# Kernel optimization log

Hardware: AMD Instinct MI355X
Metric: run time of the kernel (lower is better)

Reference implementation:

```python
import jax, jax.numpy as jnp
import numpy as np

B, S, D, UNITS = 8, 2048, 512, 512

def setup_inputs() -> dict:
    key = jax.random.key(0)
    k1, k2, k3, k4, k5 = jax.random.split(key, 5)
    inputs = jax.random.normal(k1, (B, S, D), dtype=jnp.float32)
    scale = 1.0 / np.sqrt(D)
    Ww = jax.random.normal(k2, (D, UNITS), dtype=jnp.float32) * scale
    Wb = jnp.zeros((UNITS,), dtype=jnp.float32)
    Uw = jax.random.normal(k3, (D, UNITS), dtype=jnp.float32) * scale
    Ub = jnp.zeros((UNITS,), dtype=jnp.float32)
    return {"inputs": inputs, "Ww": Ww, "Wb": Wb, "Uw": Uw, "Ub": Ub}

def reference(inputs, Ww, Wb, Uw, Ub):
    # query/key projections: [B,S,units]
    query = jnp.einsum('bsd,du->bsu', inputs, Ww) + Wb
    key_ = jnp.einsum('bsd,du->bsu', inputs, Uw) + Ub
    # unscaled scores [B,S,S], softmax over last axis
    scores = jnp.einsum('bqu,bku->bqk', query, key_)
    attn = jax.nn.softmax(scores, axis=-1)
    # context uses raw inputs as values
    context = jnp.einsum('bqk,bkd->bqd', attn, inputs)
    return context
```

## Files before the change

kernel.cpp:

```cpp
#include <hip/hip_runtime.h>
#include <stdint.h>

#define B_ 8
#define S_ 2048
#define D_ 512
#define U_ 512
#define M_TOTAL (B_*S_)
#define NPROJ (2*U_)
#define QBLK 64
#define KVBLK 64
#define NIT (S_/KVBLK)

typedef __attribute__((ext_vector_type(8))) _Float16 f16x8;
typedef __attribute__((ext_vector_type(4))) float f32x4;

__device__ __forceinline__ uint16_t f2h(float f){
  return __builtin_bit_cast(uint16_t, (_Float16)f);
}

__device__ __forceinline__ void gload16(const void* g, void* l){
  __builtin_amdgcn_global_load_lds(
      (const __attribute__((address_space(1))) void*)g,
      (__attribute__((address_space(3))) void*)l, 16, 0, 0);
}

template<int ROWS>
__device__ __forceinline__ void stage_half(char* lbase, const uint16_t* __restrict__ gpanel,
                                           int ld, int wv, int lane){
  int r0 = wv*8 + (lane>>3);
  int gs = ((lane&7) ^ (r0&7)) << 3;
  gload16(gpanel + (size_t)r0*ld + gs, lbase + wv*1024);
  if constexpr (ROWS==128){
    gload16(gpanel + (size_t)(r0+64)*ld + gs, lbase + 8192 + wv*1024);
  }
}

__global__ __launch_bounds__(256) void prep_w(const float* __restrict__ Ww,
                                              const float* __restrict__ Uw,
                                              uint16_t* __restrict__ WT){
  int idx = blockIdx.x*256 + threadIdx.x;
  int u = idx >> 9;
  int d = idx & 511;
  float v = (u < U_) ? Ww[d*U_ + u] : Uw[d*U_ + (u-U_)];
  WT[idx] = f2h(v);
}

__global__ __launch_bounds__(256) void prep_x(const float* __restrict__ X,
                                              uint16_t* __restrict__ Xf,
                                              uint16_t* __restrict__ XT){
  __shared__ float tile[32][33];
  int b = blockIdx.z;
  int s0 = blockIdx.x * 32;
  int d0 = blockIdx.y * 32;
  int tid = threadIdx.x;
  int tr = tid >> 5;
  int tc = tid & 31;
  const float* Xb = X + (size_t)b*S_*D_;
#pragma unroll
  for (int i = 0; i < 32; i += 8){
    size_t off = (size_t)(s0+tr+i)*D_ + d0+tc;
    float v = Xb[off];
    tile[tr+i][tc] = v;
    Xf[(size_t)b*S_*D_ + off] = f2h(v);
  }
  __syncthreads();
  uint16_t* XTb = XT + (size_t)b*D_*S_;
#pragma unroll
  for (int i = 0; i < 32; i += 8)
    XTb[(size_t)(d0+tr+i)*S_ + s0+tc] = f2h(tile[tc][tr+i]);
}

__global__ __launch_bounds__(512, 2) void gemm_proj(
    const uint16_t* __restrict__ A, int lda,
    const uint16_t* __restrict__ Bp, int ldb,
    uint16_t* __restrict__ Qo, uint16_t* __restrict__ Ko,
    const float* __restrict__ biasW, const float* __restrict__ biasU,
    int KD)
{
  constexpr int BMH   = 128;
  constexpr int MFR   = 8;
  constexpr int AHALF = BMH*128;
  constexpr int BHALF = 128*128;
  constexpr int DSTR  = 2*AHALF + 2*BHALF;
  __shared__ __align__(16) char smem[2*DSTR];

  const int m0 = blockIdx.y * 256;
  const int n0 = blockIdx.x * 256;
  const uint16_t* Apan = A  + (size_t)m0*lda;
  const uint16_t* Bpan = Bp + (size_t)n0*ldb;

  const int t512 = threadIdx.x;
  const int wv   = t512 >> 6;
  const int lane = t512 & 63;
  const int wm   = wv >> 2;
  const int wn   = wv & 3;
  const int fr   = lane & 15;
  const int fg   = lane >> 4;
  const int sw   = fr & 7;

  const int NT = KD >> 6;

  auto Aslot = [&](int par, int h){ return smem + par*DSTR + h*AHALF; };
  auto Bslot = [&](int par, int h){ return smem + par*DSTR + 2*AHALF + h*BHALF; };

  stage_half<128>(Aslot(0,0), Apan,                   lda, wv, lane);
  stage_half<128>(Aslot(0,1), Apan + (size_t)128*lda, lda, wv, lane);
  stage_half<128>(Bslot(0,0), Bpan,                   ldb, wv, lane);
  stage_half<128>(Bslot(0,1), Bpan + (size_t)128*ldb, ldb, wv, lane);
  if (NT > 1)
    stage_half<128>(Aslot(1,0), Apan + 64,            lda, wv, lane);
  asm volatile("s_waitcnt vmcnt(2)" ::: "memory");
  __builtin_amdgcn_s_barrier();

  f32x4 acc[MFR][4];
#pragma unroll
  for (int i=0;i<MFR;i++)
#pragma unroll
    for (int j=0;j<4;j++) acc[i][j] = (f32x4){0.f,0.f,0.f,0.f};

  for (int t = 0; t < NT; ++t){
    const int p = t & 1;
    const char* myA = Aslot(p, wm);
    const char* myB = Bslot(p, wn>>1);
    f16x8 af[MFR];

    auto rdA = [&](int ks){
#pragma unroll
      for (int mf=0; mf<MFR; ++mf)
        af[mf] = *(const f16x8*)(myA + (mf*16+fr)*128 + (((ks<<2)|fg) ^ sw)*16);
    };
    auto rdB = [&](int ks, int nh, f16x8& b0, f16x8& b1){
      int rb = (wn&1)*64 + nh*32 + fr;
      b0 = *(const f16x8*)(myB + rb*128      + (((ks<<2)|fg) ^ sw)*16);
      b1 = *(const f16x8*)(myB + (rb+16)*128 + (((ks<<2)|fg) ^ sw)*16);
    };
    auto mm = [&](int nh, f16x8 b0, f16x8 b1){
      __builtin_amdgcn_s_setprio(1);
#pragma unroll
      for (int mf=0; mf<MFR; ++mf){
        acc[mf][nh*2]   = __builtin_amdgcn_mfma_f32_16x16x32_f16(af[mf], b0, acc[mf][nh*2],   0,0,0);
        acc[mf][nh*2+1] = __builtin_amdgcn_mfma_f32_16x16x32_f16(af[mf], b1, acc[mf][nh*2+1], 0,0,0);
      }
      __builtin_amdgcn_s_setprio(0);
    };

    f16x8 b0, b1;
    rdA(0); rdB(0, 0, b0, b1);
    if (t+1 < NT)
      stage_half<128>(Aslot(p^1,1), Apan + (size_t)128*lda + (t+1)*64, lda, wv, lane);
    __builtin_amdgcn_s_barrier();
    mm(0, b0, b1);
    __builtin_amdgcn_s_barrier();
    rdB(0, 1, b0, b1);
    if (t+1 < NT)
      stage_half<128>(Bslot(p^1,0), Bpan + (t+1)*64, ldb, wv, lane);
    __builtin_amdgcn_s_barrier();
    mm(1, b0, b1);
    __builtin_amdgcn_s_barrier();
    rdA(1); rdB(1, 0, b0, b1);
    if (t+1 < NT)
      stage_half<128>(Bslot(p^1,1), Bpan + (size_t)128*ldb + (t+1)*64, ldb, wv, lane);
    __builtin_amdgcn_s_barrier();
    mm(0, b0, b1);
    __builtin_amdgcn_s_barrier();
    rdB(1, 1, b0, b1);
    if (t+2 < NT)
      stage_half<128>(Aslot(p,0), Apan + (t+2)*64, lda, wv, lane);
    __builtin_amdgcn_s_barrier();
    mm(1, b0, b1);
    asm volatile("s_waitcnt vmcnt(2)" ::: "memory");
    __builtin_amdgcn_s_barrier();
  }

#pragma unroll
  for (int mf=0; mf<MFR; ++mf)
#pragma unroll
    for (int nf=0; nf<4; ++nf){
      int col  = n0 + wn*64 + nf*16 + fr;
      int rowb = m0 + wm*128 + mf*16 + fg*4;
      f32x4 a = acc[mf][nf];
      float bias = (col < U_) ? biasW[col] : biasU[col - U_];
      if (col < U_){
#pragma unroll
        for (int r=0;r<4;r++) Qo[(size_t)(rowb+r)*U_ + col] = f2h(a[r] + bias);
      } else {
#pragma unroll
        for (int r=0;r<4;r++) Ko[(size_t)(rowb+r)*U_ + col - U_] = f2h(a[r] + bias);
      }
    }
}

__global__ __launch_bounds__(512, 2) void flash_attn(
    const uint16_t* __restrict__ Qf,
    const uint16_t* __restrict__ Kf,
    const uint16_t* __restrict__ XT,
    float* __restrict__ Out)
{
  __shared__ __align__(16) uint16_t Ks[KVBLK][512];
  __shared__ __align__(16) uint16_t Vs[512][KVBLK];
  __shared__ __align__(16) float    Ss[QBLK][68];
  __shared__ __align__(16) uint16_t Ps[QBLK][KVBLK];
  __shared__ float m_s[QBLK], l_s[QBLK], f_s[QBLK];

  const int bid   = blockIdx.x;
  const int batch = bid & 7;
  const int mblk  = bid >> 3;
  const int s0    = mblk * QBLK;

  const int t    = threadIdx.x;
  const int wv   = t >> 6;
  const int lane = t & 63;
  const int fr   = lane & 15;
  const int fg   = lane >> 4;
  const int qg = wv >> 1;
  const int kh = wv & 1;
  const int wm = wv >> 2;
  const int wd = wv & 3;

  const uint16_t* Qrow = Qf + ((size_t)batch*S_ + s0)*U_;
  const uint16_t* Krow = Kf + (size_t)batch*S_*U_;
  const uint16_t* Vt   = XT + (size_t)batch*D_*S_;

  f16x8 qreg[16];
#pragma unroll
  for (int kk=0; kk<16; ++kk)
    qreg[kk] = *(const f16x8*)(Qrow + (size_t)(qg*16+fr)*U_ + kk*32 + fg*8);

  auto stageK = [&](int ti){
    const uint16_t* src = Krow + (size_t)(ti*KVBLK)*U_;
#pragma unroll
    for (int i=0;i<8;++i){
      int r = i*8 + wv;
      gload16(src + (size_t)r*U_ + ((lane ^ (r&7))<<3),
              (char*)Ks + i*8192 + wv*1024);
    }
  };
  auto stageV = [&](int ti){
    const uint16_t* src = Vt + ti*KVBLK;
#pragma unroll
    for (int i=0;i<8;++i){
      int d = i*64 + wv*8 + (lane>>3);
      int g = lane & 7;
      gload16(src + (size_t)d*S_ + ((g ^ (d&7))<<3),
              (char*)Vs + i*8192 + wv*1024);
    }
  };

  stageK(0);
  if (t < QBLK){ m_s[t] = -3e38f; l_s[t] = 0.f; }
  f32x4 acc[2][8];
#pragma unroll
  for (int i=0;i<2;i++)
#pragma unroll
    for (int j=0;j<8;j++) acc[i][j] = (f32x4){0.f,0.f,0.f,0.f};
  asm volatile("s_waitcnt lgkmcnt(0)" ::: "memory");
  __builtin_amdgcn_s_barrier();

  for (int it=0; it<NIT; ++it){
    stageV(it);
    asm volatile("s_waitcnt vmcnt(8)" ::: "memory");

    f32x4 sfr0 = (f32x4){0.f,0.f,0.f,0.f};
    f32x4 sfr1 = (f32x4){0.f,0.f,0.f,0.f};
    __builtin_amdgcn_s_setprio(1);
#pragma unroll
    for (int kk=0; kk<16; ++kk){
      int gA = kk*4 + fg;
      int kr0 = kh*32 + fr;
      int kr1 = kh*32 + 16 + fr;
      f16x8 bv0 = *(const f16x8*)((const char*)Ks + kr0*1024 + ((gA ^ (kr0&7))<<4));
      f16x8 bv1 = *(const f16x8*)((const char*)Ks + kr1*1024 + ((gA ^ (kr1&7))<<4));
      sfr0 = __builtin_amdgcn_mfma_f32_16x16x32_f16(qreg[kk], bv0, sfr0, 0,0,0);
      sfr1 = __builtin_amdgcn_mfma_f32_16x16x32_f16(qreg[kk], bv1, sfr1, 0,0,0);
    }
    __builtin_amdgcn_s_setprio(0);
#pragma unroll
    for (int r=0;r<4;++r){
      Ss[qg*16 + fg*4 + r][kh*32 + fr]      = sfr0[r];
      Ss[qg*16 + fg*4 + r][kh*32 + 16 + fr] = sfr1[r];
    }
    asm volatile("s_waitcnt lgkmcnt(0)" ::: "memory");
    __builtin_amdgcn_s_barrier();

    {
      const int r = t >> 3, j = t & 7;
      float4 v0 = *(const float4*)&Ss[r][j*8];
      float4 v1 = *(const float4*)&Ss[r][j*8+4];
      float pm = fmaxf(fmaxf(fmaxf(v0.x,v0.y),fmaxf(v0.z,v0.w)),
                       fmaxf(fmaxf(v1.x,v1.y),fmaxf(v1.z,v1.w)));
      pm = fmaxf(pm, __shfl_xor(pm, 1));
      pm = fmaxf(pm, __shfl_xor(pm, 2));
      pm = fmaxf(pm, __shfl_xor(pm, 4));
      float mo = m_s[r];
      float mn = (pm > mo + 8.f) ? pm : mo;
      float p0 = __expf(v0.x-mn), p1 = __expf(v0.y-mn), p2 = __expf(v0.z-mn), p3 = __expf(v0.w-mn);
      float p4 = __expf(v1.x-mn), p5 = __expf(v1.y-mn), p6 = __expf(v1.z-mn), p7 = __expf(v1.w-mn);
      float sum = ((p0+p1)+(p2+p3)) + ((p4+p5)+(p6+p7));
      sum += __shfl_xor(sum, 1);
      sum += __shfl_xor(sum, 2);
      sum += __shfl_xor(sum, 4);
      if (j == 0){
        float f = __expf(mo - mn);
        f_s[r] = f;
        m_s[r] = mn;
        l_s[r] = l_s[r]*f + sum;
      }
      f16x8 pv;
      pv[0]=(_Float16)p0; pv[1]=(_Float16)p1; pv[2]=(_Float16)p2; pv[3]=(_Float16)p3;
      pv[4]=(_Float16)p4; pv[5]=(_Float16)p5; pv[6]=(_Float16)p6; pv[7]=(_Float16)p7;
      *(f16x8*)((char*)Ps + r*128 + ((j ^ (r&7))<<4)) = pv;
    }
    asm volatile("s_waitcnt lgkmcnt(0)" ::: "memory");
    __builtin_amdgcn_s_barrier();

    asm volatile("s_waitcnt vmcnt(0)" ::: "memory");
    if (it+1 < NIT) stageK(it+1);

    float fx[2][4];
#pragma unroll
    for (int mf=0; mf<2; ++mf)
#pragma unroll
      for (int r=0; r<4; ++r)
        fx[mf][r] = f_s[wm*32 + mf*16 + fg*4 + r];
    bool nr = (fx[0][0]!=1.f)|(fx[0][1]!=1.f)|(fx[0][2]!=1.f)|(fx[0][3]!=1.f)|
              (fx[1][0]!=1.f)|(fx[1][1]!=1.f)|(fx[1][2]!=1.f)|(fx[1][3]!=1.f);
    if (__any(nr)){
#pragma unroll
      for (int mf=0; mf<2; ++mf)
#pragma unroll
        for (int nf=0; nf<8; ++nf)
#pragma unroll
          for (int r=0; r<4; ++r)
            acc[mf][nf][r] *= fx[mf][r];
    }

    __builtin_amdgcn_s_setprio(1);
#pragma unroll
    for (int ks=0; ks<2; ++ks){
      int gP = ks*4 + fg;
      int q0 = wm*32 + fr;
      int q1 = wm*32 + 16 + fr;
      f16x8 pa0 = *(const f16x8*)((const char*)Ps + q0*128 + ((gP ^ (q0&7))<<4));
      f16x8 pa1 = *(const f16x8*)((const char*)Ps + q1*128 + ((gP ^ (q1&7))<<4));
#pragma unroll
      for (int nf=0; nf<8; ++nf){
        int d = wd*128 + nf*16 + fr;
        f16x8 bv = *(const f16x8*)((const char*)Vs + d*128 + ((gP ^ (d&7))<<4));
        acc[0][nf] = __builtin_amdgcn_mfma_f32_16x16x32_f16(pa0, bv, acc[0][nf], 0,0,0);
        acc[1][nf] = __builtin_amdgcn_mfma_f32_16x16x32_f16(pa1, bv, acc[1][nf], 0,0,0);
      }
    }
    __builtin_amdgcn_s_setprio(0);
    __builtin_amdgcn_s_barrier();
  }

  float linv[2][4];
#pragma unroll
  for (int mf=0; mf<2; ++mf)
#pragma unroll
    for (int r=0; r<4; ++r)
      linv[mf][r] = 1.0f / l_s[wm*32 + mf*16 + fg*4 + r];
  float* Ob = Out + ((size_t)batch*S_ + s0)*D_;
#pragma unroll
  for (int mf=0; mf<2; ++mf)
#pragma unroll
    for (int nf=0; nf<8; ++nf){
      int d = wd*128 + nf*16 + fr;
#pragma unroll
      for (int r=0; r<4; ++r){
        int q = wm*32 + mf*16 + fg*4 + r;
        Ob[(size_t)q*D_ + d] = acc[mf][nf][r] * linv[mf][r];
      }
    }
}

extern "C" void kernel_launch(void* const* d_in, const int* in_sizes, int n_in,
                              void* d_out, int out_size, void* d_ws, size_t ws_size,
                              hipStream_t stream)
{
  (void)in_sizes; (void)n_in; (void)out_size; (void)ws_size;
  const float* X  = (const float*)d_in[0];
  const float* Ww = (const float*)d_in[1];
  const float* Wb = (const float*)d_in[2];
  const float* Uw = (const float*)d_in[3];
  const float* Ub = (const float*)d_in[4];
  float* out = (float*)d_out;

  char* ws = (char*)d_ws;
  size_t off = 0;
  uint16_t* Xf = (uint16_t*)(ws + off); off += (size_t)M_TOTAL*D_*2;
  uint16_t* XT = (uint16_t*)(ws + off); off += (size_t)B_*D_*S_*2;
  uint16_t* WT = (uint16_t*)(ws + off); off += (size_t)NPROJ*D_*2;
  uint16_t* Qf = (uint16_t*)(ws + off); off += (size_t)M_TOTAL*U_*2;
  uint16_t* Kf = (uint16_t*)(ws + off); off += (size_t)M_TOTAL*U_*2;

  prep_w<<<dim3((NPROJ*D_)/256), 256, 0, stream>>>(Ww, Uw, WT);
  prep_x<<<dim3(S_/32, D_/32, B_), 256, 0, stream>>>(X, Xf, XT);

  gemm_proj<<<dim3(NPROJ/256, M_TOTAL/256, 1), 512, 0, stream>>>(
      Xf, D_, WT, D_, Qf, Kf, Wb, Ub, D_);

  flash_attn<<<dim3(B_ * (S_/QBLK)), 512, 0, stream>>>(Qf, Kf, XT, out);
}
```

Baseline: 161.2 us.

## Restructure flash-attention warp tiling, pipeline K/V prefetch, and use exp2 softmax

Folds log2(e) into the Q projection so the softmax can use native exp2, with the rescale threshold adjusted to match. Reassigns warp work: for QK^T each warp keeps two Q tiles in registers and shares a single K fragment load between them; for PV each warp owns 64 output columns across all 64 query rows, so each V fragment is reused four times. K and V staging is moved earlier in the iteration so the next tile loads while the current one computes, with sched_barriers to hold the order. The costs are higher register pressure from the larger Q and accumulator sets, and an extra barrier per iteration. The wrap-around modulo also issues one redundant prefetch at the end of the loop.

```diff
diff --git a/kernel.cpp b/kernel.cpp
--- a/kernel.cpp
+++ b/kernel.cpp
@@ -10,6 +10,7 @@
 #define QBLK 64
 #define KVBLK 64
 #define NIT (S_/KVBLK)
+#define LOG2E 1.4426950408889634f
 
 typedef __attribute__((ext_vector_type(8))) _Float16 f16x8;
 typedef __attribute__((ext_vector_type(4))) float f32x4;
@@ -182,7 +183,7 @@
       float bias = (col < U_) ? biasW[col] : biasU[col - U_];
       if (col < U_){
 #pragma unroll
-        for (int r=0;r<4;r++) Qo[(size_t)(rowb+r)*U_ + col] = f2h(a[r] + bias);
+        for (int r=0;r<4;r++) Qo[(size_t)(rowb+r)*U_ + col] = f2h((a[r] + bias)*LOG2E);
       } else {
 #pragma unroll
         for (int r=0;r<4;r++) Ko[(size_t)(rowb+r)*U_ + col - U_] = f2h(a[r] + bias);
@@ -204,27 +205,31 @@
 
   const int bid   = blockIdx.x;
   const int batch = bid & 7;
-  const int mblk  = bid >> 3;
-  const int s0    = mblk * QBLK;
+  const int s0    = (bid >> 3) * QBLK;
 
   const int t    = threadIdx.x;
   const int wv   = t >> 6;
   const int lane = t & 63;
   const int fr   = lane & 15;
   const int fg   = lane >> 4;
-  const int qg = wv >> 1;
-  const int kh = wv & 1;
-  const int wm = wv >> 2;
-  const int wd = wv & 3;
-
-  const uint16_t* Qrow = Qf + ((size_t)batch*S_ + s0)*U_;
+  const int qh   = wv >> 2;
+  const int kh   = wv & 3;
+  const int wd   = wv;
+  const int srow = wv*8 + (lane & 7);
+  const int sj   = lane >> 3;
+
   const uint16_t* Krow = Kf + (size_t)batch*S_*U_;
   const uint16_t* Vt   = XT + (size_t)batch*D_*S_;
 
-  f16x8 qreg[16];
-#pragma unroll
-  for (int kk=0; kk<16; ++kk)
-    qreg[kk] = *(const f16x8*)(Qrow + (size_t)(qg*16+fr)*U_ + kk*32 + fg*8);
+  f16x8 qreg[2][16];
+  {
+    const uint16_t* Qbase = Qf + ((size_t)batch*S_ + s0 + qh*32)*U_;
+#pragma unroll
+    for (int ti=0; ti<2; ++ti)
+#pragma unroll
+      for (int kk=0; kk<16; ++kk)
+        qreg[ti][kk] = *(const f16x8*)(Qbase + (size_t)(ti*16+fr)*U_ + kk*32 + fg*8);
+  }
 
   auto stageK = [&](int ti){
     const uint16_t* src = Krow + (size_t)(ti*KVBLK)*U_;
@@ -248,128 +253,149 @@
 
   stageK(0);
   if (t < QBLK){ m_s[t] = -3e38f; l_s[t] = 0.f; }
-  f32x4 acc[2][8];
-#pragma unroll
-  for (int i=0;i<2;i++)
-#pragma unroll
-    for (int j=0;j<8;j++) acc[i][j] = (f32x4){0.f,0.f,0.f,0.f};
-  asm volatile("s_waitcnt lgkmcnt(0)" ::: "memory");
+  stageV(0);
+  f32x4 acc[4][4];
+#pragma unroll
+  for (int i=0;i<4;i++)
+#pragma unroll
+    for (int j=0;j<4;j++) acc[i][j] = (f32x4){0.f,0.f,0.f,0.f};
+  asm volatile("s_waitcnt lgkmcnt(0) vmcnt(8)" ::: "memory");
   __builtin_amdgcn_s_barrier();
+  __builtin_amdgcn_sched_barrier(0);
 
   for (int it=0; it<NIT; ++it){
-    stageV(it);
-    asm volatile("s_waitcnt vmcnt(8)" ::: "memory");
-
-    f32x4 sfr0 = (f32x4){0.f,0.f,0.f,0.f};
-    f32x4 sfr1 = (f32x4){0.f,0.f,0.f,0.f};
-    __builtin_amdgcn_s_setprio(1);
-#pragma unroll
-    for (int kk=0; kk<16; ++kk){
-      int gA = kk*4 + fg;
-      int kr0 = kh*32 + fr;
-      int kr1 = kh*32 + 16 + fr;
-      f16x8 bv0 = *(const f16x8*)((const char*)Ks + kr0*1024 + ((gA ^ (kr0&7))<<4));
-      f16x8 bv1 = *(const f16x8*)((const char*)Ks + kr1*1024 + ((gA ^ (kr1&7))<<4));
-      sfr0 = __builtin_amdgcn_mfma_f32_16x16x32_f16(qreg[kk], bv0, sfr0, 0,0,0);
-      sfr1 = __builtin_amdgcn_mfma_f32_16x16x32_f16(qreg[kk], bv1, sfr1, 0,0,0);
-    }
-    __builtin_amdgcn_s_setprio(0);
-#pragma unroll
-    for (int r=0;r<4;++r){
-      Ss[qg*16 + fg*4 + r][kh*32 + fr]      = sfr0[r];
-      Ss[qg*16 + fg*4 + r][kh*32 + 16 + fr] = sfr1[r];
-    }
+    f32x4 sfr[2];
+    sfr[0] = (f32x4){0.f,0.f,0.f,0.f};
+    sfr[1] = (f32x4){0.f,0.f,0.f,0.f};
+    {
+      const int krow = kh*16 + fr;
+      const char* Kb = (const char*)Ks + krow*1024;
+      const int swz = krow & 7;
+      __builtin_amdgcn_s_setprio(1);
+#pragma unroll
+      for (int kk=0; kk<16; ++kk){
+        f16x8 bv = *(const f16x8*)(Kb + (((kk<<2)|fg) ^ swz)*16);
+        sfr[0] = __builtin_amdgcn_mfma_f32_16x16x32_f16(qreg[0][kk], bv, sfr[0], 0,0,0);
+        sfr[1] = __builtin_amdgcn_mfma_f32_16x16x32_f16(qreg[1][kk], bv, sfr[1], 0,0,0);
+      }
+      __builtin_amdgcn_s_setprio(0);
+    }
+#pragma unroll
+    for (int ti=0; ti<2; ++ti)
+#pragma unroll
+      for (int r=0;r<4;++r)
+        Ss[qh*32 + ti*16 + fg*4 + r][kh*16 + fr] = sfr[ti][r];
     asm volatile("s_waitcnt lgkmcnt(0)" ::: "memory");
     __builtin_amdgcn_s_barrier();
+    __builtin_amdgcn_sched_barrier(0);
+
+    stageK((it+1) & (NIT-1));
 
     {
-      const int r = t >> 3, j = t & 7;
-      float4 v0 = *(const float4*)&Ss[r][j*8];
-      float4 v1 = *(const float4*)&Ss[r][j*8+4];
+      float4 v0 = *(const float4*)&Ss[srow][sj*8];
+      float4 v1 = *(const float4*)&Ss[srow][sj*8+4];
       float pm = fmaxf(fmaxf(fmaxf(v0.x,v0.y),fmaxf(v0.z,v0.w)),
                        fmaxf(fmaxf(v1.x,v1.y),fmaxf(v1.z,v1.w)));
-      pm = fmaxf(pm, __shfl_xor(pm, 1));
-      pm = fmaxf(pm, __shfl_xor(pm, 2));
-      pm = fmaxf(pm, __shfl_xor(pm, 4));
-      float mo = m_s[r];
-      float mn = (pm > mo + 8.f) ? pm : mo;
-      float p0 = __expf(v0.x-mn), p1 = __expf(v0.y-mn), p2 = __expf(v0.z-mn), p3 = __expf(v0.w-mn);
-      float p4 = __expf(v1.x-mn), p5 = __expf(v1.y-mn), p6 = __expf(v1.z-mn), p7 = __expf(v1.w-mn);
+      pm = fmaxf(pm, __shfl_xor(pm, 8));
+      pm = fmaxf(pm, __shfl_xor(pm, 16));
+      pm = fmaxf(pm, __shfl_xor(pm, 32));
+      float mo = m_s[srow];
+      float mn = (pm > mo + 11.54f) ? pm : mo;
+      float p0 = __builtin_amdgcn_exp2f(v0.x-mn), p1 = __builtin_amdgcn_exp2f(v0.y-mn);
+      float p2 = __builtin_amdgcn_exp2f(v0.z-mn), p3 = __builtin_amdgcn_exp2f(v0.w-mn);
+      float p4 = __builtin_amdgcn_exp2f(v1.x-mn), p5 = __builtin_amdgcn_exp2f(v1.y-mn);
+      float p6 = __builtin_amdgcn_exp2f(v1.z-mn), p7 = __builtin_amdgcn_exp2f(v1.w-mn);
       float sum = ((p0+p1)+(p2+p3)) + ((p4+p5)+(p6+p7));
-      sum += __shfl_xor(sum, 1);
-      sum += __shfl_xor(sum, 2);
-      sum += __shfl_xor(sum, 4);
-      if (j == 0){
-        float f = __expf(mo - mn);
-        f_s[r] = f;
-        m_s[r] = mn;
-        l_s[r] = l_s[r]*f + sum;
-      }
-      f16x8 pv;
-      pv[0]=(_Float16)p0; pv[1]=(_Float16)p1; pv[2]=(_Float16)p2; pv[3]=(_Float16)p3;
-      pv[4]=(_Float16)p4; pv[5]=(_Float16)p5; pv[6]=(_Float16)p6; pv[7]=(_Float16)p7;
-      *(f16x8*)((char*)Ps + r*128 + ((j ^ (r&7))<<4)) = pv;
-    }
-    asm volatile("s_waitcnt lgkmcnt(0)" ::: "memory");
-    __builtin_amdgcn_s_barrier();
-
-    asm volatile("s_waitcnt vmcnt(0)" ::: "memory");
-    if (it+1 < NIT) stageK(it+1);
-
-    float fx[2][4];
-#pragma unroll
-    for (int mf=0; mf<2; ++mf)
-#pragma unroll
-      for (int r=0; r<4; ++r)
-        fx[mf][r] = f_s[wm*32 + mf*16 + fg*4 + r];
-    bool nr = (fx[0][0]!=1.f)|(fx[0][1]!=1.f)|(fx[0][2]!=1.f)|(fx[0][3]!=1.f)|
-              (fx[1][0]!=1.f)|(fx[1][1]!=1.f)|(fx[1][2]!=1.f)|(fx[1][3]!=1.f);
-    if (__any(nr)){
-#pragma unroll
-      for (int mf=0; mf<2; ++mf)
-#pragma unroll
-        for (int nf=0; nf<8; ++nf)
-#pragma unroll
-          for (int r=0; r<4; ++r)
-            acc[mf][nf][r] *= fx[mf][r];
+      sum += __shfl_xor(sum, 8);
+      sum += __shfl_xor(sum, 16);
+      sum += __shfl_xor(sum, 32);
+      if (sj == 0){
+        float f = __builtin_amdgcn_exp2f(mo - mn);
+        f_s[srow] = f;
+        m_s[srow] = mn;
+        l_s[srow] = l_s[srow]*f + sum;
+      }
+      uint32_t w0 = (uint32_t)f2h(p0) | ((uint32_t)f2h(p1)<<16);
+      uint32_t w1 = (uint32_t)f2h(p2) | ((uint32_t)f2h(p3)<<16);
+      uint32_t w2 = (uint32_t)f2h(p4) | ((uint32_t)f2h(p5)<<16);
+      uint32_t w3 = (uint32_t)f2h(p6) | ((uint32_t)f2h(p7)<<16);
+      uint4 pw = make_uint4(w0,w1,w2,w3);
+      *(uint4*)((char*)Ps + srow*128 + ((sj ^ (srow&7))<<4)) = pw;
+    }
+    asm volatile("s_waitcnt lgkmcnt(0) vmcnt(8)" ::: "memory");
+    __builtin_amdgcn_s_barrier();
+    __builtin_amdgcn_sched_barrier(0);
+
+    {
+      float fx[4][4];
+#pragma unroll
+      for (int qt=0; qt<4; ++qt)
+#pragma unroll
+        for (int r=0; r<4; ++r)
+          fx[qt][r] = f_s[qt*16 + fg*4 + r];
+      bool nr = false;
+#pragma unroll
+      for (int qt=0; qt<4; ++qt)
+#pragma unroll
+        for (int r=0; r<4; ++r) nr = nr | (fx[qt][r] != 1.f);
+      if (__any(nr)){
+#pragma unroll
+        for (int qt=0; qt<4; ++qt)
+#pragma unroll
+          for (int dt=0; dt<4; ++dt)
+#pragma unroll
+            for (int r=0; r<4; ++r)
+              acc[qt][dt][r] *= fx[qt][r];
+      }
     }
 
     __builtin_amdgcn_s_setprio(1);
 #pragma unroll
     for (int ks=0; ks<2; ++ks){
-      int gP = ks*4 + fg;
-      int q0 = wm*32 + fr;
-      int q1 = wm*32 + 16 + fr;
-      f16x8 pa0 = *(const f16x8*)((const char*)Ps + q0*128 + ((gP ^ (q0&7))<<4));
-      f16x8 pa1 = *(const f16x8*)((const char*)Ps + q1*128 + ((gP ^ (q1&7))<<4));
-#pragma unroll
-      for (int nf=0; nf<8; ++nf){
-        int d = wd*128 + nf*16 + fr;
-        f16x8 bv = *(const f16x8*)((const char*)Vs + d*128 + ((gP ^ (d&7))<<4));
-        acc[0][nf] = __builtin_amdgcn_mfma_f32_16x16x32_f16(pa0, bv, acc[0][nf], 0,0,0);
-        acc[1][nf] = __builtin_amdgcn_mfma_f32_16x16x32_f16(pa1, bv, acc[1][nf], 0,0,0);
-      }
+      f16x8 pa[4], bv[4];
+#pragma unroll
+      for (int qt=0; qt<4; ++qt){
+        int q = qt*16 + fr;
+        pa[qt] = *(const f16x8*)((const char*)Ps + q*128 + ((((ks<<2)|fg) ^ (q&7))<<4));
+      }
+#pragma unroll
+      for (int dt=0; dt<4; ++dt){
+        int d = wd*64 + dt*16 + fr;
+        bv[dt] = *(const f16x8*)((const char*)Vs + d*128 + ((((ks<<2)|fg) ^ (d&7))<<4));
+      }
+#pragma unroll
+      for (int qt=0; qt<4; ++qt)
+#pragma unroll
+        for (int dt=0; dt<4; ++dt)
+          acc[qt][dt] = __builtin_amdgcn_mfma_f32_16x16x32_f16(pa[qt], bv[dt], acc[qt][dt], 0,0,0);
     }
     __builtin_amdgcn_s_setprio(0);
-    __builtin_amdgcn_s_barrier();
+    asm volatile("" ::: "memory");
+    __builtin_amdgcn_s_barrier();
+    __builtin_amdgcn_sched_barrier(0);
+
+    stageV((it+1) & (NIT-1));
+    asm volatile("s_waitcnt vmcnt(8)" ::: "memory");
+    __builtin_amdgcn_s_barrier();
+    __builtin_amdgcn_sched_barrier(0);
   }
 
-  float linv[2][4];
-#pragma unroll
-  for (int mf=0; mf<2; ++mf)
+  float linv[4][4];
+#pragma unroll
+  for (int qt=0; qt<4; ++qt)
 #pragma unroll
     for (int r=0; r<4; ++r)
-      linv[mf][r] = 1.0f / l_s[wm*32 + mf*16 + fg*4 + r];
+      linv[qt][r] = 1.0f / l_s[qt*16 + fg*4 + r];
   float* Ob = Out + ((size_t)batch*S_ + s0)*D_;
 #pragma unroll
-  for (int mf=0; mf<2; ++mf)
-#pragma unroll
-    for (int nf=0; nf<8; ++nf){
-      int d = wd*128 + nf*16 + fr;
+  for (int qt=0; qt<4; ++qt)
+#pragma unroll
+    for (int dt=0; dt<4; ++dt){
+      int d = wd*64 + dt*16 + fr;
 #pragma unroll
       for (int r=0; r<4; ++r){
-        int q = wm*32 + mf*16 + fg*4 + r;
-        Ob[(size_t)q*D_ + d] = acc[mf][nf][r] * linv[mf][r];
+        int q = qt*16 + fg*4 + r;
+        Ob[(size_t)q*D_ + d] = acc[qt][dt][r] * linv[qt][r];
       }
     }
 }
```

Result: slower. 202.8 us (+25.8%).
